# Kernel tuning notes

Hardware: AMD Instinct MI355X
Metric: run time of the kernel (lower is better)

## Reference

```python
import jax, jax.numpy as jnp
import numpy as np
import math

JOINT_DIM = 16
D_MODEL = 128
NUM_HEADS = 8
HEAD_DIM = D_MODEL // NUM_HEADS


def kinematic_adjacency():
    adj = np.zeros((JOINT_DIM, JOINT_DIM), dtype=np.float32)
    skeleton = [(0, 1), (1, 2), (2, 3), (0, 4), (4, 5), (5, 6), (0, 7), (7, 8),
                (8, 9), (0, 10), (10, 11), (11, 12), (0, 13), (13, 14), (14, 15)]
    for p, c in skeleton:
        adj[p, c] = 1.0
        adj[c, p] = 1.0
    sym = [(4, 7), (5, 8), (6, 9), (10, 13), (11, 14), (12, 15)]
    for a, b in sym:
        adj[a, b] += 0.8
        adj[b, a] += 0.8
    adj += np.eye(JOINT_DIM, dtype=np.float32)
    return jnp.asarray(adj)


def setup_inputs() -> dict:
    key = jax.random.key(0)
    ks = jax.random.split(key, 9)
    B, S = 64, 512
    s3 = 1.0 / math.sqrt(3.0)
    sd = 1.0 / math.sqrt(D_MODEL)
    return {
        "x": jax.random.normal(ks[0], (B, S, JOINT_DIM, 3), dtype=jnp.float32),
        "Wq": jax.random.uniform(ks[1], (3, D_MODEL), jnp.float32, -s3, s3),
        "bq": jax.random.uniform(ks[2], (D_MODEL,), jnp.float32, -s3, s3),
        "Wk": jax.random.uniform(ks[3], (3, D_MODEL), jnp.float32, -s3, s3),
        "bk": jax.random.uniform(ks[4], (D_MODEL,), jnp.float32, -s3, s3),
        "Wv": jax.random.uniform(ks[5], (3, D_MODEL), jnp.float32, -s3, s3),
        "bv": jax.random.uniform(ks[6], (D_MODEL,), jnp.float32, -s3, s3),
        "Wo": jax.random.uniform(ks[7], (D_MODEL, D_MODEL), jnp.float32, -sd, sd),
        "bo": jax.random.uniform(ks[8], (D_MODEL,), jnp.float32, -sd, sd),
    }


def reference(x, Wq, bq, Wk, bk, Wv, bv, Wo, bo):
    B, S, J, _ = x.shape
    adj = kinematic_adjacency()  # [J, J]

    def split_heads(t):  # [B,S,J,D] -> [B,S,H,J,hd]
        return t.reshape(B, S, J, NUM_HEADS, HEAD_DIM).transpose(0, 1, 3, 2, 4)

    q = split_heads(x @ Wq + bq)
    k = split_heads(x @ Wk + bk)
    v = split_heads(x @ Wv + bv)

    # scores get adjacency bias BEFORE the 1/sqrt(head_dim) scaling (as in source)
    scores = jnp.einsum('bshjd,bshkd->bshjk', q, k)
    scores = (scores + adj) / math.sqrt(HEAD_DIM)
    w = jax.nn.softmax(scores, axis=-1)  # dropout inactive (eval)
    ctx = jnp.einsum('bshjk,bshkd->bshjd', w, v)
    ctx = ctx.transpose(0, 1, 3, 2, 4).reshape(B, S, J, D_MODEL)
    return ctx @ Wo + bo  # [B,S,J,D]
```

## Files before the change

### kernel.cpp

```cpp
#include <hip/hip_runtime.h>

#define NJ   16
#define DM   128
#define NH   8
#define P    8
#define CL   0.36067376022224085f

typedef __attribute__((ext_vector_type(8))) short bf16x8;
typedef __attribute__((ext_vector_type(4))) float f32x4;

__constant__ float c_adj[NJ * NJ] = {
    1,1,0,0, 1,0,0,1, 0,0,1,0, 0,1,0,0,
    1,1,1,0, 0,0,0,0, 0,0,0,0, 0,0,0,0,
    0,1,1,1, 0,0,0,0, 0,0,0,0, 0,0,0,0,
    0,0,1,1, 0,0,0,0, 0,0,0,0, 0,0,0,0,
    1,0,0,0, 1,1,0,0.8f, 0,0,0,0, 0,0,0,0,
    0,0,0,0, 1,1,1,0, 0.8f,0,0,0, 0,0,0,0,
    0,0,0,0, 0,1,1,0, 0,0.8f,0,0, 0,0,0,0,
    1,0,0,0, 0.8f,0,0,1, 1,0,0,0, 0,0,0,0,
    0,0,0,0, 0,0.8f,0,1, 1,1,0,0, 0,0,0,0,
    0,0,0,0, 0,0,0.8f,0, 1,1,0,0, 0,0,0,0,
    1,0,0,0, 0,0,0,0, 0,0,1,1, 0,0.8f,0,0,
    0,0,0,0, 0,0,0,0, 0,0,1,1, 1,0,0.8f,0,
    0,0,0,0, 0,0,0,0, 0,0,0,1, 1,0,0,0.8f,
    1,0,0,0, 0,0,0,0, 0,0,0.8f,0, 0,1,1,0,
    0,0,0,0, 0,0,0,0, 0,0,0,0.8f, 0,1,1,1,
    0,0,0,0, 0,0,0,0, 0,0,0,0, 0.8f,0,1,1
};

#define WS_BP_W   0
#define WS_PACK_W 128
#define WS_GF_W   256

__device__ __forceinline__ unsigned short f2bf(float f) {
    union { float f; unsigned u; } v; v.f = f;
    unsigned u = v.u;
    u += 0x7FFFu + ((u >> 16) & 1u);
    return (unsigned short)(u >> 16);
}
__device__ __forceinline__ unsigned pack2bf(float lo, float hi) {
    return (unsigned)f2bf(lo) | ((unsigned)f2bf(hi) << 16);
}

__global__ __launch_bounds__(256) void skel_setup_kernel(
    const float* __restrict__ Wq, const float* __restrict__ bq,
    const float* __restrict__ Wk, const float* __restrict__ bk,
    const float* __restrict__ Wv, const float* __restrict__ bv,
    const float* __restrict__ Wo, const float* __restrict__ bo,
    unsigned* __restrict__ wsu)
{
    const int b = blockIdx.x, t = threadIdx.x;
    float* wsf = (float*)wsu;

    if (b < 8) {
        const int idx = b * 256 + t;
        const int ctl = idx >> 2, i = idx & 3;
        const int ct = ctl >> 6, l = ctl & 63;
        const int n  = ct * 16 + (l & 15);
        const int kb = (l >> 4) * 8;
        float v[2];
#pragma unroll
        for (int s = 0; s < 2; ++s) {
            const int k = kb + 2 * i + s;
            const int h = k >> 2, r = k & 3;
            float acc = 0.f;
            if (r < 3) {
#pragma unroll
                for (int dh = 0; dh < 16; ++dh)
                    acc += Wv[r * DM + h * 16 + dh] * Wo[(h * 16 + dh) * DM + n];
            }
            v[s] = acc;
        }
        wsu[WS_GF_W + idx] = pack2bf(v[0], v[1]);
        return;
    }
    if (t < 128) {
        const int n = t;
        float bv_ = bo[n];
        for (int d = 0; d < DM; ++d) bv_ += bv[d] * Wo[d * DM + n];
        wsf[WS_BP_W + n] = bv_;
    } else if (t < 128 + NH) {
        const int h = t - 128;
        float* o = &wsf[WS_PACK_W + h * 16];
#pragma unroll
        for (int r = 0; r < 3; ++r)
#pragma unroll
            for (int c = 0; c < 3; ++c) {
                float acc = 0.f;
#pragma unroll
                for (int dh = 0; dh < 16; ++dh)
                    acc += Wq[r * DM + h * 16 + dh] * Wk[c * DM + h * 16 + dh];
                o[r * 3 + c] = acc * CL;
            }
#pragma unroll
        for (int r = 0; r < 3; ++r) {
            float aa = 0.f, cc = 0.f;
#pragma unroll
            for (int dh = 0; dh < 16; ++dh) {
                aa += Wq[r * DM + h * 16 + dh] * bk[h * 16 + dh];
                cc += Wk[r * DM + h * 16 + dh] * bq[h * 16 + dh];
            }
            o[9 + r]  = aa * CL;
            o[12 + r] = cc * CL;
        }
        float dd = 0.f;
#pragma unroll
        for (int dh = 0; dh < 16; ++dh) dd += bq[h * 16 + dh] * bk[h * 16 + dh];
        o[15] = dd * CL;
    }
}

__global__ __launch_bounds__(256) void skel_main_kernel(
    const float* __restrict__ x,
    const unsigned* __restrict__ wsu,
    float* __restrict__ out,
    int npos)
{
    const int t = threadIdx.x;
    const long pos0 = (long)blockIdx.x * P;
    const float* wsf = (const float*)wsu;

    __shared__ __align__(16) float    sx4[P][NJ][4];
    __shared__ float                  sc[128];
    __shared__ __align__(16) unsigned sxb[4][NJ * 20];
    __shared__ __align__(16) float    sbp[128];
    __shared__ __align__(16) float    sout[4][NJ * DM];

    if (t < 128) {
        const int p = t >> 4, j = t & 15;
        const long pidx = pos0 + p;
        const long base = pidx * 48 + j * 3;
        const bool ok = pidx < npos;
        sx4[p][j][0] = ok ? x[base + 0] : 0.f;
        sx4[p][j][1] = ok ? x[base + 1] : 0.f;
        sx4[p][j][2] = ok ? x[base + 2] : 0.f;
        sx4[p][j][3] = 0.f;
    } else {
        const int i = t - 128;
        sc[i]  = wsf[WS_PACK_W + i];
        sbp[i] = wsf[WS_BP_W + i];
    }
    __syncthreads();

    const int wv = t >> 6, l = t & 63;
    const int h  = l >> 3, j0 = l & 7;
    const int jB = l & 15, lkB = l >> 4;

    bf16x8 ga[8];
#pragma unroll
    for (int ct = 0; ct < 8; ++ct)
        ga[ct] = *(const bf16x8*)&wsu[WS_GF_W + (ct * 64 + l) * 4];

    float m[16];
#pragma unroll
    for (int i = 0; i < 16; ++i) m[i] = sc[h * 16 + i];
    float adj0[NJ], adj1[NJ];
#pragma unroll
    for (int k = 0; k < NJ; ++k) {
        adj0[k] = c_adj[j0 * NJ + k] * CL;
        adj1[k] = c_adj[(j0 + 8) * NJ + k] * CL;
    }

    float* so = &sout[wv][0];

    for (int it = 0; it < 2; ++it) {
        const int p = wv * 2 + it;
        const f32x4 xa = *(const f32x4*)&sx4[p][j0];
        const f32x4 xb = *(const f32x4*)&sx4[p][j0 + 8];

        const float y00 = m[0]*xa.x + m[3]*xa.y + m[6]*xa.z + m[12];
        const float y01 = m[1]*xa.x + m[4]*xa.y + m[7]*xa.z + m[13];
        const float y02 = m[2]*xa.x + m[5]*xa.y + m[8]*xa.z + m[14];
        const float u0  = m[9]*xa.x + m[10]*xa.y + m[11]*xa.z + m[15];
        const float y10 = m[0]*xb.x + m[3]*xb.y + m[6]*xb.z + m[12];
        const float y11 = m[1]*xb.x + m[4]*xb.y + m[7]*xb.z + m[13];
        const float y12 = m[2]*xb.x + m[5]*xb.y + m[8]*xb.z + m[14];
        const float u1  = m[9]*xb.x + m[10]*xb.y + m[11]*xb.z + m[15];

        float sum0 = 0.f, sum1 = 0.f;
        float a00 = 0.f, a01 = 0.f, a02 = 0.f;
        float a10 = 0.f, a11 = 0.f, a12 = 0.f;
#pragma unroll
        for (int k = 0; k < NJ; ++k) {
            const f32x4 xk = *(const f32x4*)&sx4[p][k];
            const float e0 = exp2f(y00*xk.x + y01*xk.y + y02*xk.z + u0 + adj0[k]);
            const float e1 = exp2f(y10*xk.x + y11*xk.y + y12*xk.z + u1 + adj1[k]);
            sum0 += e0; sum1 += e1;
            a00 += e0 * xk.x; a01 += e0 * xk.y; a02 += e0 * xk.z;
            a10 += e1 * xk.x; a11 += e1 * xk.y; a12 += e1 * xk.z;
        }
        const float inv0 = __builtin_amdgcn_rcpf(sum0);
        const float inv1 = __builtin_amdgcn_rcpf(sum1);

        {
            uint2 w0, w1;
            w0.x = pack2bf(a00 * inv0, a01 * inv0);
            w0.y = pack2bf(a02 * inv0, 0.f);
            w1.x = pack2bf(a10 * inv1, a11 * inv1);
            w1.y = pack2bf(a12 * inv1, 0.f);
            *(uint2*)&sxb[wv][j0 * 20 + 2 * h]       = w0;
            *(uint2*)&sxb[wv][(j0 + 8) * 20 + 2 * h] = w1;
        }
        const bf16x8 bvec = *(const bf16x8*)&sxb[wv][jB * 20 + lkB * 4];

#pragma unroll
        for (int ct = 0; ct < 8; ++ct) {
            f32x4 acc = *(const f32x4*)&sbp[ct * 16 + lkB * 4];
            acc = __builtin_amdgcn_mfma_f32_16x16x32_bf16(ga[ct], bvec, acc, 0, 0, 0);
            *(f32x4*)&so[jB * 128 + (((ct * 4 + lkB) ^ (jB & 7)) << 2)] = acc;
        }

        if (pos0 + p < npos) {
            float* ob = out + (pos0 + p) * (long)(NJ * DM);
#pragma unroll
            for (int c2 = 0; c2 < 8; ++c2) {
                const int jR = c2 * 2 + (l >> 5);
                const int ul = l & 31;
                const f32x4 vq = *(const f32x4*)&so[jR * 128 + ((ul ^ (jR & 7)) << 2)];
                *(f32x4*)(ob + c2 * 256 + l * 4) = vq;
            }
        }
    }
}

extern "C" void kernel_launch(void* const* d_in, const int* in_sizes, int n_in,
                              void* d_out, int out_size, void* d_ws, size_t ws_size,
                              hipStream_t stream) {
    const float* x  = (const float*)d_in[0];
    const float* Wq = (const float*)d_in[1];
    const float* bq = (const float*)d_in[2];
    const float* Wk = (const float*)d_in[3];
    const float* bk = (const float*)d_in[4];
    const float* Wv = (const float*)d_in[5];
    const float* bv = (const float*)d_in[6];
    const float* Wo = (const float*)d_in[7];
    const float* bo = (const float*)d_in[8];
    float* out    = (float*)d_out;
    unsigned* wsu = (unsigned*)d_ws;

    const int npos = in_sizes[0] / (NJ * 3);
    skel_setup_kernel<<<9, 256, 0, stream>>>(Wq, bq, Wk, bk, Wv, bv, Wo, bo, wsu);
    const int grid = (npos + P - 1) / P;
    skel_main_kernel<<<grid, 256, 0, stream>>>(x, wsu, out, npos);
}
```

Baseline: 66.26 us.

## Shrink LDS output staging and move per-lane constants to shared memory for occupancy

The main kernel now stages its output through a smaller double-buffered shared tile, one 32-column slice per pair of MFMAs, instead of a full 16x128 tile per wave. The adjacency and per-head constants are read from padded shared arrays inside the loop rather than held in registers, and the launch bound asks for 5 blocks per CU. The gf fragment load is also moved before the barrier. The aim is to cut register and LDS use so more waves can run at once, at the cost of extra LDS reads in the inner softmax loop and narrower 128-byte global store segments.

```diff
diff --git a/kernel.cpp b/kernel.cpp
--- a/kernel.cpp
+++ b/kernel.cpp
@@ -110,7 +110,7 @@
     }
 }
 
-__global__ __launch_bounds__(256) void skel_main_kernel(
+__global__ __launch_bounds__(256, 5) void skel_main_kernel(
     const float* __restrict__ x,
     const unsigned* __restrict__ wsu,
     float* __restrict__ out,
@@ -121,11 +121,13 @@
     const float* wsf = (const float*)wsu;
 
     __shared__ __align__(16) float    sx4[P][NJ][4];
-    __shared__ float                  sc[128];
+    __shared__ float                  sc[NH][17];
+    __shared__ float                  sadj[NJ][17];
+    __shared__ __align__(16) float    sbp[128];
     __shared__ __align__(16) unsigned sxb[4][NJ * 20];
-    __shared__ __align__(16) float    sbp[128];
-    __shared__ __align__(16) float    sout[4][NJ * DM];
-
+    __shared__ __align__(16) float    sout[4][2][NJ*32];
+
+    sadj[t >> 4][t & 15] = c_adj[t] * CL;
     if (t < 128) {
         const int p = t >> 4, j = t & 15;
         const long pidx = pos0 + p;
@@ -137,45 +139,40 @@
         sx4[p][j][3] = 0.f;
     } else {
         const int i = t - 128;
-        sc[i]  = wsf[WS_PACK_W + i];
+        sc[i >> 4][i & 15] = wsf[WS_PACK_W + i];
         sbp[i] = wsf[WS_BP_W + i];
     }
+    const int l = t & 63;
+    bf16x8 ga[8];
+#pragma unroll
+    for (int ct = 0; ct < 8; ++ct)
+        ga[ct] = *(const bf16x8*)&wsu[WS_GF_W + (ct * 64 + l) * 4];
     __syncthreads();
 
-    const int wv = t >> 6, l = t & 63;
+    const int wv = t >> 6;
     const int h  = l >> 3, j0 = l & 7;
     const int jB = l & 15, lkB = l >> 4;
-
-    bf16x8 ga[8];
-#pragma unroll
-    for (int ct = 0; ct < 8; ++ct)
-        ga[ct] = *(const bf16x8*)&wsu[WS_GF_W + (ct * 64 + l) * 4];
-
-    float m[16];
-#pragma unroll
-    for (int i = 0; i < 16; ++i) m[i] = sc[h * 16 + i];
-    float adj0[NJ], adj1[NJ];
-#pragma unroll
-    for (int k = 0; k < NJ; ++k) {
-        adj0[k] = c_adj[j0 * NJ + k] * CL;
-        adj1[k] = c_adj[(j0 + 8) * NJ + k] * CL;
-    }
-
-    float* so = &sout[wv][0];
+    const int rS = l >> 3, uS = l & 7;
 
     for (int it = 0; it < 2; ++it) {
         const int p = wv * 2 + it;
         const f32x4 xa = *(const f32x4*)&sx4[p][j0];
         const f32x4 xb = *(const f32x4*)&sx4[p][j0 + 8];
 
-        const float y00 = m[0]*xa.x + m[3]*xa.y + m[6]*xa.z + m[12];
-        const float y01 = m[1]*xa.x + m[4]*xa.y + m[7]*xa.z + m[13];
-        const float y02 = m[2]*xa.x + m[5]*xa.y + m[8]*xa.z + m[14];
-        const float u0  = m[9]*xa.x + m[10]*xa.y + m[11]*xa.z + m[15];
-        const float y10 = m[0]*xb.x + m[3]*xb.y + m[6]*xb.z + m[12];
-        const float y11 = m[1]*xb.x + m[4]*xb.y + m[7]*xb.z + m[13];
-        const float y12 = m[2]*xb.x + m[5]*xb.y + m[8]*xb.z + m[14];
-        const float u1  = m[9]*xb.x + m[10]*xb.y + m[11]*xb.z + m[15];
+        const float m0 = sc[h][0],  m1 = sc[h][1],  m2 = sc[h][2];
+        const float m3 = sc[h][3],  m4 = sc[h][4],  m5 = sc[h][5];
+        const float m6 = sc[h][6],  m7 = sc[h][7],  m8 = sc[h][8];
+        const float m9 = sc[h][9],  mA = sc[h][10], mB = sc[h][11];
+        const float mC = sc[h][12], mD = sc[h][13], mE = sc[h][14], mF = sc[h][15];
+
+        const float y00 = m0*xa.x + m3*xa.y + m6*xa.z + mC;
+        const float y01 = m1*xa.x + m4*xa.y + m7*xa.z + mD;
+        const float y02 = m2*xa.x + m5*xa.y + m8*xa.z + mE;
+        const float u0  = m9*xa.x + mA*xa.y + mB*xa.z + mF;
+        const float y10 = m0*xb.x + m3*xb.y + m6*xb.z + mC;
+        const float y11 = m1*xb.x + m4*xb.y + m7*xb.z + mD;
+        const float y12 = m2*xb.x + m5*xb.y + m8*xb.z + mE;
+        const float u1  = m9*xb.x + mA*xb.y + mB*xb.z + mF;
 
         float sum0 = 0.f, sum1 = 0.f;
         float a00 = 0.f, a01 = 0.f, a02 = 0.f;
@@ -183,8 +180,10 @@
 #pragma unroll
         for (int k = 0; k < NJ; ++k) {
             const f32x4 xk = *(const f32x4*)&sx4[p][k];
-            const float e0 = exp2f(y00*xk.x + y01*xk.y + y02*xk.z + u0 + adj0[k]);
-            const float e1 = exp2f(y10*xk.x + y11*xk.y + y12*xk.z + u1 + adj1[k]);
+            const float ad0 = sadj[j0][k];
+            const float ad1 = sadj[j0 + 8][k];
+            const float e0 = exp2f(y00*xk.x + y01*xk.y + y02*xk.z + (u0 + ad0));
+            const float e1 = exp2f(y10*xk.x + y11*xk.y + y12*xk.z + (u1 + ad1));
             sum0 += e0; sum1 += e1;
             a00 += e0 * xk.x; a01 += e0 * xk.y; a02 += e0 * xk.z;
             a10 += e1 * xk.x; a11 += e1 * xk.y; a12 += e1 * xk.z;
@@ -203,21 +202,26 @@
         }
         const bf16x8 bvec = *(const bf16x8*)&sxb[wv][jB * 20 + lkB * 4];
 
-#pragma unroll
-        for (int ct = 0; ct < 8; ++ct) {
-            f32x4 acc = *(const f32x4*)&sbp[ct * 16 + lkB * 4];
-            acc = __builtin_amdgcn_mfma_f32_16x16x32_bf16(ga[ct], bvec, acc, 0, 0, 0);
-            *(f32x4*)&so[jB * 128 + (((ct * 4 + lkB) ^ (jB & 7)) << 2)] = acc;
-        }
-
-        if (pos0 + p < npos) {
-            float* ob = out + (pos0 + p) * (long)(NJ * DM);
-#pragma unroll
-            for (int c2 = 0; c2 < 8; ++c2) {
-                const int jR = c2 * 2 + (l >> 5);
-                const int ul = l & 31;
-                const f32x4 vq = *(const f32x4*)&so[jR * 128 + ((ul ^ (jR & 7)) << 2)];
-                *(f32x4*)(ob + c2 * 256 + l * 4) = vq;
+        const bool ok = (pos0 + p) < npos;
+        float* ob = out + (pos0 + p) * (long)(NJ * DM);
+
+#pragma unroll
+        for (int pr = 0; pr < 4; ++pr) {
+            float* sb = &sout[wv][pr & 1][0];
+
+            f32x4 acc0 = *(const f32x4*)&sbp[(2*pr)   * 16 + lkB * 4];
+            f32x4 acc1 = *(const f32x4*)&sbp[(2*pr+1) * 16 + lkB * 4];
+            acc0 = __builtin_amdgcn_mfma_f32_16x16x32_bf16(ga[2*pr],   bvec, acc0, 0, 0, 0);
+            acc1 = __builtin_amdgcn_mfma_f32_16x16x32_bf16(ga[2*pr+1], bvec, acc1, 0, 0, 0);
+
+            *(f32x4*)&sb[jB * 32 + (( lkB      ) ^ (jB & 7)) * 4] = acc0;
+            *(f32x4*)&sb[jB * 32 + (( 4 + lkB  ) ^ (jB & 7)) * 4] = acc1;
+
+            if (ok) {
+                const f32x4 v1 = *(const f32x4*)&sb[ rS      * 32 + (uS ^ ( rS      & 7)) * 4];
+                const f32x4 v2 = *(const f32x4*)&sb[(rS + 8) * 32 + (uS ^ ((rS + 8) & 7)) * 4];
+                *(f32x4*)(ob +  rS      * DM + pr * 32 + uS * 4) = v1;
+                *(f32x4*)(ob + (rS + 8) * DM + pr * 32 + uS * 4) = v2;
             }
         }
     }
```

Result: slower. 70.10 us (+5.8%).
